# Kernel optimization log

Measured on AMD Instinct MI355X. Metric: run time of the kernel, lower is better.

Reference implementation:

```python
import jax, jax.numpy as jnp
import numpy as np

S, N, C = 16384, 2048, 8  # n_samples, n_channels, n_components

def setup_inputs() -> dict:
    key = jax.random.key(0)
    k1, k2, k3, k4 = jax.random.split(key, 4)
    return {
        "inputs": jax.random.uniform(k1, (S, N), dtype=jnp.float32),
        "components": jax.random.uniform(k2, (C, N), dtype=jnp.float32),
        "contributions": jax.random.uniform(k3, (S, C), dtype=jnp.float32),
        "shift": jax.random.normal(k4, (S, C), dtype=jnp.float32) * 3.0,
    }

def reference(inputs, components, contributions, shift):
    # fit_shift=True branch. The original builds k_matrix[i,j] = j - i and
    # coeff[i,j] = clip(1 - |shift - (j - i)|, 0, 1), then dots with the
    # component. That is exactly linear interpolation of component at
    # position i + shift, with zero padding outside [0, N-1].
    n_samples, n_channels = inputs.shape
    n_comp = components.shape[0]
    i = jnp.arange(n_channels, dtype=shift.dtype)
    pos = i[None, None, :] + shift[:, :, None]            # [S, C, N]
    j0f = jnp.floor(pos)
    frac = pos - j0f                                      # in [0, 1)
    j0 = j0f.astype(jnp.int32)
    j1 = j0 + 1
    cidx = jnp.arange(n_comp)[None, :, None]              # broadcast over [S, C, N]
    g0 = components[cidx, jnp.clip(j0, 0, n_channels - 1)]
    g1 = components[cidx, jnp.clip(j1, 0, n_channels - 1)]
    v0 = ((j0 >= 0) & (j0 < n_channels)).astype(components.dtype)
    v1 = ((j1 >= 0) & (j1 < n_channels)).astype(components.dtype)
    shifted = g0 * (1.0 - frac) * v0 + g1 * frac * v1     # [S, C, N] shifted components
    # scale by per-sample contributions and sum over components
    return jnp.einsum('scn,sc->sn', shifted, contributions)
```

## Files before the change

### kernel.cpp

```cpp
#include <hip/hip_runtime.h>
#include <hip/hip_fp16.h>


namespace {
constexpr int kS = 16384;
constexpr int kN = 2048;
constexpr int kC = 8;
constexpr int kK = 320;
constexpr int kSlots = 40;
constexpr size_t kGtBytes = (size_t)kN * kK * 2;
constexpr size_t kWsNeed  = kGtBytes;

typedef _Float16 f16x8 __attribute__((ext_vector_type(8)));
typedef float    f32x4 __attribute__((ext_vector_type(4)));

__global__ __launch_bounds__(256)
void buildG_kernel(const float* __restrict__ comps, __half* __restrict__ Gt) {
    const int tid = blockIdx.x * 256 + threadIdx.x;
    const int c = tid >> 11;
    const int n = tid & 2047;
    const float* src = comps + c * kN;

    uint32_t w[kSlots / 2];
    #pragma unroll
    for (int t2 = 0; t2 < kSlots / 2; ++t2) {
        uint32_t pk = 0;
        #pragma unroll
        for (int h = 0; h < 2; ++h) {
            const int t = 2 * t2 + h;
            float v = 0.f;
            if (t < 35) {
                const int j = n + (t - 17);
                if (j >= 0 && j < kN) v = src[j];
            }
            const __half hv = __float2half_rn(v);
            pk |= (uint32_t)__half_as_ushort(hv) << (16 * h);
        }
        w[t2] = pk;
    }
    uint4* dst = reinterpret_cast<uint4*>(Gt + (size_t)n * kK + c * kSlots);
    #pragma unroll
    for (int i = 0; i < kSlots / 8; ++i)
        dst[i] = make_uint4(w[4 * i], w[4 * i + 1], w[4 * i + 2], w[4 * i + 3]);
}

__global__ __launch_bounds__(512, 2)
void gemm_kernel(const float* __restrict__ contrib,
                 const float* __restrict__ shift,
                 const __half* __restrict__ Gt,
                 float* __restrict__ out)
{
    __shared__ __half Atile[64 * kK];
    __shared__ __half Btile[128 * kK];
    __shared__ float  outB[64 * 136];

    const int tid = threadIdx.x;
    const int s0  = blockIdx.x * 64;

    const int rr = tid >> 2;
    const int sb = tid & 3;
    const int xw = rr & 7;
    uint4 tb[10];
    {
        const __half* g = Gt + (size_t)rr * kK;
        #pragma unroll
        for (int q = 0; q < 10; ++q)
            tb[q] = *reinterpret_cast<const uint4*>(g + (sb + 4 * q) * 8);
    }

    #pragma unroll
    for (int i = 0; i < 5; ++i)
        reinterpret_cast<uint4*>(Atile)[i * 512 + tid] = make_uint4(0u,0u,0u,0u);
    __syncthreads();
    {
        const int sr = tid >> 3;
        const int c  = tid & 7;
        const float ctv = contrib[(size_t)(s0 + sr) * kC + c];
        const float sv  = shift[(size_t)(s0 + sr) * kC + c];
        int d = (int)floorf(sv);
        d = d < -17 ? -17 : (d > 16 ? 16 : d);
        const float fr = sv - (float)d;
        const __half w1h = __float2half_rn(ctv * fr);
        const __half w0h = __float2half_rn(ctv - __half2float(w1h));
        const int h0 = c * kSlots + d + 17;
        const int h1 = h0 + 1;
        const int x  = sr & 7;
        Atile[sr * kK + (((h0 >> 3) ^ x) << 3) + (h0 & 7)] = w0h;
        Atile[sr * kK + (((h1 >> 3) ^ x) << 3) + (h1 & 7)] = w1h;
    }
    __syncthreads();

    const int lane = tid & 63;
    const int wave = tid >> 6;
    const int wm = (wave >> 2) * 32;
    const int wn = (wave & 3) * 32;
    const int l15 = lane & 15, l4 = lane >> 4;

    f16x8 af[10][2];
    #pragma unroll
    for (int mi = 0; mi < 2; ++mi) {
        const int r = wm + mi * 16 + l15;
        const int x = r & 7;
        #pragma unroll
        for (int ks = 0; ks < 10; ++ks) {
            const int sl = (ks * 4 + l4) ^ x;
            af[ks][mi] = *reinterpret_cast<const f16x8*>(&Atile[r * kK + sl * 8]);
        }
    }

    const int rB0 = wn + l15, rB1 = rB0 + 16;
    const int xB0 = rB0 & 7,  xB1 = rB1 & 7;
    const int bBase0 = rB0 * kK, bBase1 = rB1 * kK;

    #pragma unroll 1
    for (int step = 0; step < 16; ++step) {
        __syncthreads();

        {
            __half* drow = Btile + rr * kK;
            #pragma unroll
            for (int q = 0; q < 10; ++q) {
                const int sl = (sb + 4 * q) ^ xw;
                *reinterpret_cast<uint4*>(drow + sl * 8) = tb[q];
            }
        }
        __syncthreads();

        if (step < 15) {
            const __half* g = Gt + ((size_t)(step + 1) * 128 + rr) * kK;
            #pragma unroll
            for (int q = 0; q < 10; ++q)
                tb[q] = *reinterpret_cast<const uint4*>(g + (sb + 4 * q) * 8);
        }

        f32x4 acc00 = {0.f,0.f,0.f,0.f}, acc01 = {0.f,0.f,0.f,0.f};
        f32x4 acc10 = {0.f,0.f,0.f,0.f}, acc11 = {0.f,0.f,0.f,0.f};
        #pragma unroll
        for (int ks = 0; ks < 10; ++ks) {
            const int kq = ks * 4 + l4;
            const f16x8 b0 = *reinterpret_cast<const f16x8*>(
                &Btile[bBase0 + ((kq ^ xB0) << 3)]);
            const f16x8 b1 = *reinterpret_cast<const f16x8*>(
                &Btile[bBase1 + ((kq ^ xB1) << 3)]);
            acc00 = __builtin_amdgcn_mfma_f32_16x16x32_f16(af[ks][0], b0, acc00, 0,0,0);
            acc01 = __builtin_amdgcn_mfma_f32_16x16x32_f16(af[ks][0], b1, acc01, 0,0,0);
            acc10 = __builtin_amdgcn_mfma_f32_16x16x32_f16(af[ks][1], b0, acc10, 0,0,0);
            acc11 = __builtin_amdgcn_mfma_f32_16x16x32_f16(af[ks][1], b1, acc11, 0,0,0);
        }

        #pragma unroll
        for (int v = 0; v < 4; ++v) {
            outB[(wm +  0 + l4*4 + v) * 136 + wn +  0 + l15] = acc00[v];
            outB[(wm +  0 + l4*4 + v) * 136 + wn + 16 + l15] = acc01[v];
            outB[(wm + 16 + l4*4 + v) * 136 + wn +  0 + l15] = acc10[v];
            outB[(wm + 16 + l4*4 + v) * 136 + wn + 16 + l15] = acc11[v];
        }
        __syncthreads();

        const int n0 = step * 128;
        #pragma unroll
        for (int k2 = 0; k2 < 4; ++k2) {
            const int f   = k2 * 512 + tid;
            const int row = f >> 5;
            const int c4  = f & 31;
            const f32x4 val = *reinterpret_cast<const f32x4*>(&outB[row * 136 + c4 * 4]);
            __builtin_nontemporal_store(val,
                reinterpret_cast<f32x4*>(out + (size_t)(s0 + row) * kN + n0 + c4 * 4));
        }
    }
}

constexpr int kMf     = 16;
constexpr int kBlockF = 512;
constexpr int kPadH  = 32;
constexpr int kUnits = 1057;
constexpr int kRowStride = 1192;
__device__ __forceinline__ int swz(int u) { return u + (u >> 3); }

__global__ __launch_bounds__(kBlockF, 8)
void smf_kernel(const float* __restrict__ comps,
                const float* __restrict__ contrib,
                const float* __restrict__ shift,
                float* __restrict__ out)
{
    __shared__ uint32_t ldsU[kC * kRowStride];
    __shared__ float    ctLds[kMf * kC];
    __shared__ float    shLds[kMf * kC];

    const int tid = threadIdx.x;
    const int s0  = blockIdx.x * kMf;

    for (int c = 0; c < kC; ++c) {
        const float* src = comps + c * kN;
        uint32_t* dstp = ldsU + c * kRowStride;
        for (int u = tid; u < kUnits; u += kBlockF) {
            const int j = 2 * u - kPadH;
            float2 v = make_float2(0.f, 0.f);
            if (j >= 0 && j < kN - 1) v = *reinterpret_cast<const float2*>(src + j);
            __half2 h2 = __floats2half2_rn(v.x, v.y);
            dstp[swz(u)] = *reinterpret_cast<const uint32_t*>(&h2);
        }
    }
    for (int tt = tid; tt < (kMf * kC) / 2; tt += kBlockF) {
        if (tt < (kMf * kC) / 4) {
            reinterpret_cast<float4*>(ctLds)[tt] =
                reinterpret_cast<const float4*>(contrib + (size_t)s0 * kC)[tt];
        } else {
            const int t2 = tt - (kMf * kC) / 4;
            reinterpret_cast<float4*>(shLds)[t2] =
                reinterpret_cast<const float4*>(shift + (size_t)s0 * kC)[t2];
        }
    }
    __syncthreads();

    const int q = tid >> 8;
    const int t = tid & 255;

    #pragma unroll 1
    for (int r = 0; r < kMf / 2; ++r) {
        const int si = q * (kMf / 2) + r;
        const int s  = s0 + si;
        const float4 ccA = *reinterpret_cast<const float4*>(ctLds + si * kC);
        const float4 ccB = *reinterpret_cast<const float4*>(ctLds + si * kC + 4);
        const float4 csA = *reinterpret_cast<const float4*>(shLds + si * kC);
        const float4 csB = *reinterpret_cast<const float4*>(shLds + si * kC + 4);
        const float ct[8] = {ccA.x, ccA.y, ccA.z, ccA.w, ccB.x, ccB.y, ccB.z, ccB.w};
        const float sh[8] = {csA.x, csA.y, csA.z, csA.w, csB.x, csB.y, csB.z, csB.w};
        float accA[4], accB[4];
        #pragma unroll
        for (int k = 0; k < 4; ++k) { accA[k] = 0.f; accB[k] = 0.f; }
        #pragma unroll
        for (int c = 0; c < kC; ++c) {
            const float fl = floorf(sh[c]);
            const float fr = sh[c] - fl;
            int d = (int)fl;
            d = d < -31 ? -31 : (d > 31 ? 31 : d);
            const float w1 = ct[c] * fr;
            const float w0 = ct[c] - w1;
            const int a   = 4 * t + d + kPadH;
            const int u0  = a >> 1;
            const bool odd = (a & 1) != 0;
            const uint32_t* row = ldsU + c * kRowStride;
            const uint32_t yA0 = row[swz(u0 + 0)];
            const uint32_t yA1 = row[swz(u0 + 1)];
            const uint32_t yA2 = row[swz(u0 + 2)];
            const uint32_t yB0 = row[swz(u0 + 512)];
            const uint32_t yB1 = row[swz(u0 + 513)];
            const uint32_t yB2 = row[swz(u0 + 514)];
            const uint32_t zA0 = odd ? __builtin_amdgcn_alignbit(yA1, yA0, 16) : yA0;
            const uint32_t zA1 = odd ? __builtin_amdgcn_alignbit(yA2, yA1, 16) : yA1;
            const uint32_t zA2 = odd ? (yA2 >> 16) : yA2;
            const uint32_t zB0 = odd ? __builtin_amdgcn_alignbit(yB1, yB0, 16) : yB0;
            const uint32_t zB1 = odd ? __builtin_amdgcn_alignbit(yB2, yB1, 16) : yB1;
            const uint32_t zB2 = odd ? (yB2 >> 16) : yB2;
            const float2 fA0 = __half22float2(*reinterpret_cast<const __half2*>(&zA0));
            const float2 fA1 = __half22float2(*reinterpret_cast<const __half2*>(&zA1));
            const float2 fA2 = __half22float2(*reinterpret_cast<const __half2*>(&zA2));
            const float2 fB0 = __half22float2(*reinterpret_cast<const __half2*>(&zB0));
            const float2 fB1 = __half22float2(*reinterpret_cast<const __half2*>(&zB1));
            const float2 fB2 = __half22float2(*reinterpret_cast<const __half2*>(&zB2));
            accA[0] += w0 * fA0.x + w1 * fA0.y;
            accA[1] += w0 * fA0.y + w1 * fA1.x;
            accA[2] += w0 * fA1.x + w1 * fA1.y;
            accA[3] += w0 * fA1.y + w1 * fA2.x;
            accB[0] += w0 * fB0.x + w1 * fB0.y;
            accB[1] += w0 * fB0.y + w1 * fB1.x;
            accB[2] += w0 * fB1.x + w1 * fB1.y;
            accB[3] += w0 * fB1.y + w1 * fB2.x;
        }
        float* orow = out + (size_t)s * kN;
        *reinterpret_cast<float4*>(orow + 4 * t) =
            make_float4(accA[0], accA[1], accA[2], accA[3]);
        *reinterpret_cast<float4*>(orow + 1024 + 4 * t) =
            make_float4(accB[0], accB[1], accB[2], accB[3]);
    }
}
}

extern "C" void kernel_launch(void* const* d_in, const int* in_sizes, int n_in,
                              void* d_out, int out_size, void* d_ws, size_t ws_size,
                              hipStream_t stream) {
    const float* comps   = (const float*)d_in[1];
    const float* contrib = (const float*)d_in[2];
    const float* shiftp  = (const float*)d_in[3];
    float* out = (float*)d_out;

    if (ws_size >= kWsNeed && d_ws != nullptr) {
        __half* Gt = (__half*)d_ws;
        buildG_kernel<<<dim3((kC * kN) / 256), dim3(256), 0, stream>>>(comps, Gt);
        gemm_kernel<<<dim3(kS / 64), dim3(512), 0, stream>>>(contrib, shiftp, Gt, out);
    } else {
        smf_kernel<<<dim3(kS / kMf), dim3(kBlockF), 0, stream>>>(comps, contrib, shiftp, out);
    }
}
```

Measured before the change: 294.2 us.

## Double-buffer B tile in the MFMA GEMM and store accumulators directly to global

```diff
diff --git a/kernel.cpp b/kernel.cpp
--- a/kernel.cpp
+++ b/kernel.cpp
@@ -51,21 +51,20 @@
                  float* __restrict__ out)
 {
     __shared__ __half Atile[64 * kK];
-    __shared__ __half Btile[128 * kK];
-    __shared__ float  outB[64 * 136];
+    __shared__ __half Btile[2][64 * kK];
 
     const int tid = threadIdx.x;
     const int s0  = blockIdx.x * 64;
 
-    const int rr = tid >> 2;
-    const int sb = tid & 3;
-    const int xw = rr & 7;
-    uint4 tb[10];
+    const int rr = tid >> 3;
+    const int sb = tid & 7;
+    uint4 tb[5];
+
     {
         const __half* g = Gt + (size_t)rr * kK;
         #pragma unroll
-        for (int q = 0; q < 10; ++q)
-            tb[q] = *reinterpret_cast<const uint4*>(g + (sb + 4 * q) * 8);
+        for (int q = 0; q < 5; ++q)
+            tb[q] = *reinterpret_cast<const uint4*>(g + (sb + 8 * q) * 8);
     }
 
     #pragma unroll
@@ -93,7 +92,7 @@
     const int lane = tid & 63;
     const int wave = tid >> 6;
     const int wm = (wave >> 2) * 32;
-    const int wn = (wave & 3) * 32;
+    const int wn = (wave & 3) * 16;
     const int l15 = lane & 15, l4 = lane >> 4;
 
     f16x8 af[10][2];
@@ -108,65 +107,72 @@
         }
     }
 
-    const int rB0 = wn + l15, rB1 = rB0 + 16;
-    const int xB0 = rB0 & 7,  xB1 = rB1 & 7;
-    const int bBase0 = rB0 * kK, bBase1 = rB1 * kK;
+    {
+        __half* drow = &Btile[0][rr * kK];
+        #pragma unroll
+        for (int q = 0; q < 5; ++q) {
+            const int sl = (sb + 8 * q) ^ (rr & 7);
+            *reinterpret_cast<uint4*>(drow + sl * 8) = tb[q];
+        }
+    }
+    {
+        const __half* g = Gt + ((size_t)64 + rr) * kK;
+        #pragma unroll
+        for (int q = 0; q < 5; ++q)
+            tb[q] = *reinterpret_cast<const uint4*>(g + (sb + 8 * q) * 8);
+    }
+    asm volatile("s_waitcnt lgkmcnt(0)" ::: "memory");
+    __builtin_amdgcn_s_barrier();
+    __builtin_amdgcn_sched_barrier(0);
+
+    const int rB = wn + l15;
+    const int xB = rB & 7;
+    const int bBase = rB * kK;
 
     #pragma unroll 1
-    for (int step = 0; step < 16; ++step) {
-        __syncthreads();
-
-        {
-            __half* drow = Btile + rr * kK;
+    for (int step = 0; step < 32; ++step) {
+        const int cur = step & 1;
+        const int nxt = cur ^ 1;
+
+        if (step < 31) {
+            __half* drow = &Btile[nxt][rr * kK];
             #pragma unroll
-            for (int q = 0; q < 10; ++q) {
-                const int sl = (sb + 4 * q) ^ xw;
+            for (int q = 0; q < 5; ++q) {
+                const int sl = (sb + 8 * q) ^ (rr & 7);
                 *reinterpret_cast<uint4*>(drow + sl * 8) = tb[q];
             }
         }
-        __syncthreads();
-
-        if (step < 15) {
-            const __half* g = Gt + ((size_t)(step + 1) * 128 + rr) * kK;
+        if (step < 30) {
+            const __half* g = Gt + ((size_t)(step + 2) * 64 + rr) * kK;
             #pragma unroll
-            for (int q = 0; q < 10; ++q)
-                tb[q] = *reinterpret_cast<const uint4*>(g + (sb + 4 * q) * 8);
-        }
-
-        f32x4 acc00 = {0.f,0.f,0.f,0.f}, acc01 = {0.f,0.f,0.f,0.f};
-        f32x4 acc10 = {0.f,0.f,0.f,0.f}, acc11 = {0.f,0.f,0.f,0.f};
+            for (int q = 0; q < 5; ++q)
+                tb[q] = *reinterpret_cast<const uint4*>(g + (sb + 8 * q) * 8);
+        }
+
+        f32x4 acc0 = {0.f,0.f,0.f,0.f};
+        f32x4 acc1 = {0.f,0.f,0.f,0.f};
         #pragma unroll
         for (int ks = 0; ks < 10; ++ks) {
             const int kq = ks * 4 + l4;
-            const f16x8 b0 = *reinterpret_cast<const f16x8*>(
-                &Btile[bBase0 + ((kq ^ xB0) << 3)]);
-            const f16x8 b1 = *reinterpret_cast<const f16x8*>(
-                &Btile[bBase1 + ((kq ^ xB1) << 3)]);
-            acc00 = __builtin_amdgcn_mfma_f32_16x16x32_f16(af[ks][0], b0, acc00, 0,0,0);
-            acc01 = __builtin_amdgcn_mfma_f32_16x16x32_f16(af[ks][0], b1, acc01, 0,0,0);
-            acc10 = __builtin_amdgcn_mfma_f32_16x16x32_f16(af[ks][1], b0, acc10, 0,0,0);
-            acc11 = __builtin_amdgcn_mfma_f32_16x16x32_f16(af[ks][1], b1, acc11, 0,0,0);
-        }
-
-        #pragma unroll
-        for (int v = 0; v < 4; ++v) {
-            outB[(wm +  0 + l4*4 + v) * 136 + wn +  0 + l15] = acc00[v];
-            outB[(wm +  0 + l4*4 + v) * 136 + wn + 16 + l15] = acc01[v];
-            outB[(wm + 16 + l4*4 + v) * 136 + wn +  0 + l15] = acc10[v];
-            outB[(wm + 16 + l4*4 + v) * 136 + wn + 16 + l15] = acc11[v];
-        }
-        __syncthreads();
-
-        const int n0 = step * 128;
-        #pragma unroll
-        for (int k2 = 0; k2 < 4; ++k2) {
-            const int f   = k2 * 512 + tid;
-            const int row = f >> 5;
-            const int c4  = f & 31;
-            const f32x4 val = *reinterpret_cast<const f32x4*>(&outB[row * 136 + c4 * 4]);
-            __builtin_nontemporal_store(val,
-                reinterpret_cast<f32x4*>(out + (size_t)(s0 + row) * kN + n0 + c4 * 4));
-        }
+            const f16x8 b = *reinterpret_cast<const f16x8*>(
+                &Btile[cur][bBase + ((kq ^ xB) << 3)]);
+            acc0 = __builtin_amdgcn_mfma_f32_16x16x32_f16(af[ks][0], b, acc0, 0,0,0);
+            acc1 = __builtin_amdgcn_mfma_f32_16x16x32_f16(af[ks][1], b, acc1, 0,0,0);
+        }
+
+        {
+            float* col = out + (size_t)(step * 64 + wn + l15);
+            const int r0 = s0 + wm + l4 * 4;
+            #pragma unroll
+            for (int v = 0; v < 4; ++v) {
+                col[(size_t)(r0 + v) * kN]      = acc0[v];
+                col[(size_t)(r0 + 16 + v) * kN] = acc1[v];
+            }
+        }
+
+        asm volatile("s_waitcnt lgkmcnt(0)" ::: "memory");
+        __builtin_amdgcn_s_barrier();
+        __builtin_amdgcn_sched_barrier(0);
     }
 }
 
```

Result: faster. 260.7 us (-11.4%).
